# Kernel optimization log

Measured on AMD Instinct MI355X. Metric: run time of the kernel, lower is better.

Reference implementation:

```python
import jax, jax.numpy as jnp
import numpy as np
from jax import lax

B, C_IN, H, W = 32, 128, 64, 64
K, C_OUT, KS = 8, 128, 3
HID = C_IN * 4  # extend = 4
TEMPERATURE = 1.0
PAD = 1


def setup_inputs() -> dict:
    key = jax.random.key(0)
    ks = jax.random.split(key, 7)
    x = jax.random.normal(ks[0], (B, C_IN, H, W), jnp.float32)
    prompt_param = jax.random.uniform(ks[1], (1, K, HID), jnp.float32)
    w1 = jax.random.normal(ks[2], (HID, C_IN), jnp.float32) * 0.05
    b1 = jnp.zeros((HID,), jnp.float32)
    w2 = jax.random.normal(ks[3], (HID, HID), jnp.float32) * 0.05
    b2 = jnp.zeros((HID,), jnp.float32)
    kernels_weights = jax.random.normal(ks[4], (K, C_OUT, C_IN, KS, KS), jnp.float32) * 0.05
    kernels_bias = jax.random.normal(ks[5], (K, C_OUT), jnp.float32) * 0.05
    return {
        'x': x, 'prompt_param': prompt_param,
        'w1': w1, 'b1': b1, 'w2': w2, 'b2': b2,
        'kernels_weights': kernels_weights, 'kernels_bias': kernels_bias,
    }


def reference(x, prompt_param, w1, b1, w2, b2, kernels_weights, kernels_bias):
    # Attention: global avg pool -> MLP -> prompt dot -> softmax over kernels
    pooled = jnp.mean(x, axis=(2, 3))                       # (B, C_in)
    h = jax.nn.relu(pooled @ w1.T + b1)                     # (B, HID)
    s = h @ w2.T + b2                                       # (B, HID)
    scores = jnp.sum(s[:, None, :] * prompt_param, axis=-1)  # (B, K)
    alphas = jax.nn.softmax(scores / TEMPERATURE, axis=-1)   # (B, K)

    # Per-sample kernel aggregation
    agg_w = jnp.einsum('bk,koihw->boihw', alphas, kernels_weights)  # (B,O,I,kh,kw)
    agg_b = alphas @ kernels_bias                                    # (B, O)

    # Per-sample conv2d (equivalent to the groups=B grouped-conv trick)
    def conv_one(xi, wi):
        # xi: (C_in,H,W), wi: (O,C_in,kh,kw)
        return lax.conv_general_dilated(
            xi[None], wi, window_strides=(1, 1),
            padding=((PAD, PAD), (PAD, PAD)),
            dimension_numbers=('NCHW', 'OIHW', 'NCHW'))[0]
    out = jax.vmap(conv_one)(x, agg_w)                       # (B,O,H,W)
    out = out + agg_b[:, :, None, None]
    return out
```

## Files before the change

### kernel.cpp

```cpp
#include <hip/hip_runtime.h>
#include <hip/hip_bf16.h>
#include <stdint.h>


typedef __bf16 v8bf __attribute__((ext_vector_type(8)));
typedef float  v4f  __attribute__((ext_vector_type(4)));

#define XT_OFF     0u
#define XT_BYTES   (32u*4096u*128u*2u)
#define AGGW_OFF   (XT_OFF + XT_BYTES)
#define AGGW_BYTES (32u*9u*128u*128u*2u)
#define PART_OFF   (AGGW_OFF)
#define POOLED_OFF (AGGW_OFF + 0x100000u)
#define H_OFF      (AGGW_OFF + 0x110000u)
#define PSCORE_OFF (AGGW_OFF + 0x120000u)
#define ALPHA_OFF  (AGGW_OFF + AGGW_BYTES)
#define ALPHA_BYTES (32u*8u*4u)
#define AGGB_OFF   (ALPHA_OFF + ALPHA_BYTES)
#define AGGB_BYTES (32u*128u*4u)

typedef const void __attribute__((address_space(1))) gconst_t;
typedef void       __attribute__((address_space(3))) ldsv_t;

__device__ __forceinline__ void g2l16(const void* g, void* l) {
  __builtin_amdgcn_global_load_lds((gconst_t*)g, (ldsv_t*)l, 16, 0, 0);
}

__global__ __launch_bounds__(256) void pool_convert_kernel(
    const float* __restrict__ x, float* __restrict__ partial,
    __hip_bfloat16* __restrict__ xT) {
  const int b = blockIdx.x >> 6;
  const int h = blockIdx.x & 63;
  const int tid = threadIdx.x;
  const int wv = tid >> 6, lane = tid & 63;
  const int wq = lane & 15;
  const int cl = lane >> 4;
  __shared__ __align__(16) __hip_bfloat16 sT[64 * 130];

  const float* xrow = x + (((size_t)b * 128) << 12) + (h << 6);
  #pragma unroll
  for (int i = 0; i < 8; ++i) {
    int c = wv * 32 + i * 4 + cl;
    float4 v = *(const float4*)&xrow[((size_t)c << 12) + wq * 4];
    int w0 = wq * 4;
    sT[(w0 + 0) * 130 + c] = __float2bfloat16(v.x);
    sT[(w0 + 1) * 130 + c] = __float2bfloat16(v.y);
    sT[(w0 + 2) * 130 + c] = __float2bfloat16(v.z);
    sT[(w0 + 3) * 130 + c] = __float2bfloat16(v.w);
    float s = v.x + v.y + v.z + v.w;
    s += __shfl_xor(s, 1);
    s += __shfl_xor(s, 2);
    s += __shfl_xor(s, 4);
    s += __shfl_xor(s, 8);
    if (wq == 0) partial[((b << 6) + h) * 128 + c] = s;
  }
  __syncthreads();
  const int pw = tid >> 2;
  const int piece = tid & 3;
  const uint32_t* s32 = (const uint32_t*)sT;
  uint32_t vals[16];
  #pragma unroll
  for (int j = 0; j < 16; ++j) vals[j] = s32[pw * 65 + piece * 16 + j];
  char* dst = (char*)xT + ((((size_t)b << 6) + h) * 64 + pw) * 256 + piece * 64;
  #pragma unroll
  for (int j = 0; j < 4; ++j)
    ((uint4*)dst)[j] = make_uint4(vals[4*j], vals[4*j+1], vals[4*j+2], vals[4*j+3]);
}

__global__ __launch_bounds__(128) void pool_reduce_kernel(
    const float* __restrict__ partial, float* __restrict__ pooled) {
  const int b = blockIdx.x, c = threadIdx.x;
  float acc = 0.0f;
  const float* src = partial + ((size_t)b << 6) * 128 + c;
  #pragma unroll 8
  for (int h = 0; h < 64; ++h) acc += src[h * 128];
  pooled[b * 128 + c] = acc * (1.0f / 4096.0f);
}

__global__ __launch_bounds__(256) void attn_l1_kernel(
    const float* __restrict__ pooled, const float* __restrict__ w1,
    const float* __restrict__ b1, float* __restrict__ hbuf) {
  const int jt = blockIdx.x * 8;
  const int tid = threadIdx.x;
  __shared__ float sW[8 * 132];
  __shared__ float sPool[32 * 132];

  {
    int r = tid >> 5, c4 = (tid & 31) * 4;
    *(float4*)&sW[r * 132 + c4] = *(const float4*)&w1[(jt + r) * 128 + c4];
  }
  #pragma unroll
  for (int q = 0; q < 4; ++q) {
    int idx = q * 256 + tid;
    int bb = idx >> 5, c4 = (idx & 31) * 4;
    *(float4*)&sPool[bb * 132 + c4] = *(const float4*)&pooled[bb * 128 + c4];
  }
  __syncthreads();

  const int b = tid >> 3, jr = tid & 7;
  float acc = 0.0f;
  #pragma unroll
  for (int i4 = 0; i4 < 32; ++i4) {
    float4 pv = *(const float4*)&sPool[b * 132 + i4 * 4];
    float4 wv = *(const float4*)&sW[jr * 132 + i4 * 4];
    acc += pv.x * wv.x + pv.y * wv.y + pv.z * wv.z + pv.w * wv.w;
  }
  hbuf[b * 512 + jt + jr] = fmaxf(acc + b1[jt + jr], 0.0f);
}

__global__ __launch_bounds__(256) void attn_l2s_kernel(
    const float* __restrict__ hbuf, const float* __restrict__ w2,
    const float* __restrict__ b2, const float* __restrict__ prompt,
    float* __restrict__ pscore) {
  const int jtile = blockIdx.x >> 1;
  const int bg = blockIdx.x & 1;
  const int jt = jtile * 8;
  const int tid = threadIdx.x;
  __shared__ float sW2[8 * 516];
  __shared__ float sH[16 * 516];
  __shared__ float sSc[16 * 9];
  __shared__ float sPr[64];

  #pragma unroll
  for (int q = 0; q < 4; ++q) {
    int idx = q * 256 + tid;
    int r = idx >> 7, c4 = (idx & 127) * 4;
    *(float4*)&sW2[r * 516 + c4] = *(const float4*)&w2[(jt + r) * 512 + c4];
  }
  #pragma unroll
  for (int q = 0; q < 8; ++q) {
    int idx = q * 256 + tid;
    int r = idx >> 7, c4 = (idx & 127) * 4;
    *(float4*)&sH[r * 516 + c4] =
        *(const float4*)&hbuf[(bg * 16 + r) * 512 + c4];
  }
  if (tid < 64) sPr[tid] = prompt[(tid >> 3) * 512 + jt + (tid & 7)];
  __syncthreads();

  const int pair = tid >> 1, half = tid & 1;
  const int bl = pair >> 3, jr = pair & 7;
  float acc = 0.0f;
  #pragma unroll
  for (int i4 = 0; i4 < 64; ++i4) {
    int idx = (half * 64 + i4) * 4;
    float4 hv = *(const float4*)&sH[bl * 516 + idx];
    float4 wv = *(const float4*)&sW2[jr * 516 + idx];
    acc += hv.x * wv.x + hv.y * wv.y + hv.z * wv.z + hv.w * wv.w;
  }
  acc += __shfl_xor(acc, 1);
  if (half == 0) sSc[bl * 9 + jr] = acc + b2[jt + jr];
  __syncthreads();

  if (tid < 128) {
    int bl = tid >> 3, k = tid & 7;
    float p = 0.0f;
    #pragma unroll
    for (int jj = 0; jj < 8; ++jj) p = fmaf(sSc[bl * 9 + jj], sPr[k * 8 + jj], p);
    pscore[((size_t)(jtile * 32 + bg * 16 + bl)) * 8 + k] = p;
  }
}

__global__ __launch_bounds__(256) void softmax_aggb_kernel(
    const float* __restrict__ pscore, const float* __restrict__ kbias,
    float* __restrict__ alphas, float* __restrict__ aggb) {
  const int b = blockIdx.x;
  const int tid = threadIdx.x;
  __shared__ float sRed[32 * 8], sSc[8], sA[8];

  {
    int jt2 = tid >> 3, k = tid & 7;
    sRed[jt2 * 8 + k] = pscore[((size_t)(jt2 * 32 + b)) * 8 + k] +
                        pscore[((size_t)((jt2 + 32) * 32 + b)) * 8 + k];
  }
  __syncthreads();
  if (tid < 8) {
    float sc = 0.0f;
    #pragma unroll
    for (int j = 0; j < 32; ++j) sc += sRed[j * 8 + tid];
    sSc[tid] = sc;
  }
  __syncthreads();
  if (tid == 0) {
    float mx = sSc[0];
    for (int k = 1; k < 8; ++k) mx = fmaxf(mx, sSc[k]);
    float sum = 0.0f, e[8];
    for (int k = 0; k < 8; ++k) { e[k] = expf(sSc[k] - mx); sum += e[k]; }
    float inv = 1.0f / sum;
    for (int k = 0; k < 8; ++k) sA[k] = e[k] * inv;
  }
  __syncthreads();
  if (tid < 8) alphas[b * 8 + tid] = sA[tid];
  if (tid < 128) {
    float acc = 0.0f;
    #pragma unroll
    for (int k = 0; k < 8; ++k) acc = fmaf(sA[k], kbias[k * 128 + tid], acc);
    aggb[b * 128 + tid] = acc;
  }
}

__global__ __launch_bounds__(128) void agg_weights_kernel(
    const float* __restrict__ kw, const float* __restrict__ alphas,
    __hip_bfloat16* __restrict__ aggw) {
  const int co = blockIdx.x;
  const int bg = blockIdx.y;
  const int tid = threadIdx.x;
  __shared__ float sA[64];
  __shared__ float sbuf[1152];
  if (tid < 64) sA[tid] = alphas[bg * 64 + tid];
  __syncthreads();

  float acc[8][9];
  #pragma unroll
  for (int bb = 0; bb < 8; ++bb)
    #pragma unroll
    for (int q = 0; q < 9; ++q) acc[bb][q] = 0.0f;

  for (int k = 0; k < 8; ++k) {
    const float* src = kw + ((size_t)(k * 128 + co)) * 1152;
    float v[9];
    #pragma unroll
    for (int q = 0; q < 9; ++q) v[q] = src[tid + 128 * q];
    #pragma unroll
    for (int bb = 0; bb < 8; ++bb) {
      float a = sA[bb * 8 + k];
      #pragma unroll
      for (int q = 0; q < 9; ++q) acc[bb][q] = fmaf(a, v[q], acc[bb][q]);
    }
  }

  #pragma unroll 1
  for (int bb = 0; bb < 8; ++bb) {
    __syncthreads();
    #pragma unroll
    for (int q = 0; q < 9; ++q) sbuf[tid + 128 * q] = acc[bb][q];
    __syncthreads();
    const int b = bg * 8 + bb;
    #pragma unroll
    for (int t = 0; t < 9; ++t)
      aggw[(((size_t)(b * 9 + t) * 128 + co) << 7) + tid] =
          __float2bfloat16(sbuf[tid * 9 + t]);
  }
}

#define XTILE_B 33792
#define ABUF_B  16384

__global__ __launch_bounds__(256) void dyn_conv_kernel(
    const __hip_bfloat16* __restrict__ xT, const __hip_bfloat16* __restrict__ aggw,
    const float* __restrict__ aggb, float* __restrict__ out) {
  const int tile = blockIdx.x;
  const int b    = blockIdx.y;
  const int tid  = threadIdx.x;
  const int wv = tid >> 6, lane = tid & 63;
  const int wm = wv >> 1, wn = wv & 1;
  const int lm = lane & 15, quad = lane >> 4;
  const int r0 = tile * 2;

  __shared__ __align__(16) char smem[XTILE_B + 2 * ABUF_B + 512];
  char* xb = smem;
  char* abuf = smem + XTILE_B;
  float* sBias = (float*)(smem + XTILE_B + 2 * ABUF_B);

  if (tid < 128) sBias[tid] = aggb[b * 128 + tid];

  for (int pos = tid; pos < 264; pos += 256) {
    int tr = pos / 66, tc = pos - tr * 66;
    int h = r0 - 1 + tr, w = tc - 1;
    if ((unsigned)h >= 64u || (unsigned)w >= 64u) {
      int4* d = (int4*)(xb + pos * 128);
      #pragma unroll
      for (int i = 0; i < 8; ++i) d[i] = make_int4(0, 0, 0, 0);
    }
  }

  const char* xTb = (const char*)xT + ((size_t)b << 20);
  const char* awb = (const char*)aggw + (size_t)b * 294912;

  auto stageX = [&](int half) {
    for (int i = wv; i < 33; i += 4) {
      int P = (i << 6) + lane;
      int pos = P >> 3, slot = P & 7;
      int tr = pos / 66, tc = pos - tr * 66;
      int h = r0 - 1 + tr, w = tc - 1;
      char* dst = xb + (i << 10);
      if ((unsigned)h < 64u && (unsigned)w < 64u) {
        int p = slot ^ (pos & 7);
        const char* src = xTb + (((h << 6) + w) << 8) + (half << 7) + (p << 4);
        g2l16(src, dst);
      }
    }
  };

  auto stageA = [&](int tap, int half) {
    char* ab = abuf + (tap & 1) * ABUF_B;
    #pragma unroll
    for (int sub = 0; sub < 2; ++sub) {
      const int cic = half * 2 + sub;
      const char* base = awb + (tap << 15) + (cic << 6);
      #pragma unroll
      for (int jj = 0; jj < 2; ++jj) {
        int j = wv * 2 + jj;
        int co = (j << 4) + (lane >> 2);
        int f = lane & 3;
        int p = f ^ ((co >> 1) & 3);
        g2l16(base + (co << 8) + (p << 4), ab + sub * 8192 + (j << 10));
      }
    }
  };

  int posb[4];
  #pragma unroll
  for (int ni = 0; ni < 4; ++ni) {
    int n = wn * 64 + ni * 16 + lm;
    posb[ni] = (n >> 6) * 66 + (n & 63);
  }
  const int fA = (quad ^ ((lm >> 1) & 3)) << 4;
  int aoff[4];
  #pragma unroll
  for (int mi = 0; mi < 4; ++mi) {
    int co = wm * 64 + mi * 16 + lm;
    aoff[mi] = (co << 6) + fA;
  }

  v4f acc[4][4];
  #pragma unroll
  for (int mi = 0; mi < 4; ++mi)
    #pragma unroll
    for (int ni = 0; ni < 4; ++ni) acc[mi][ni] = v4f{0.f, 0.f, 0.f, 0.f};

  auto computeTap = [&](int tap) {
    const int th = tap / 3, tw = tap - th * 3;
    const int tapAdd = th * 66 + tw;
    char* ab = abuf + (tap & 1) * ABUF_B;
    #pragma unroll
    for (int sub = 0; sub < 2; ++sub) {
      v8bf af[4], bfr[4];
      #pragma unroll
      for (int mi = 0; mi < 4; ++mi)
        af[mi] = *(const v8bf*)(ab + sub * 8192 + aoff[mi]);
      const int piece = (sub << 2) | quad;
      #pragma unroll
      for (int ni = 0; ni < 4; ++ni) {
        int pos = posb[ni] + tapAdd;
        int pp = (piece ^ (pos & 7)) << 4;
        bfr[ni] = *(const v8bf*)(xb + (pos << 7) + pp);
      }
      #pragma unroll
      for (int mi = 0; mi < 4; ++mi)
        #pragma unroll
        for (int ni = 0; ni < 4; ++ni)
          acc[mi][ni] = __builtin_amdgcn_mfma_f32_16x16x32_bf16(
              af[mi], bfr[ni], acc[mi][ni], 0, 0, 0);
    }
  };

  stageA(0, 0);
  stageA(1, 0);
  stageX(0);
  __syncthreads();
  #pragma unroll
  for (int tap = 0; tap < 9; ++tap) {
    computeTap(tap);
    __syncthreads();
    if (tap + 2 < 9) stageA(tap + 2, 0);
  }
  stageX(1);
  stageA(0, 1);
  stageA(1, 1);
  __syncthreads();
  #pragma unroll
  for (int tap = 0; tap < 9; ++tap) {
    computeTap(tap);
    if (tap < 8) {
      __syncthreads();
      if (tap + 2 < 9) stageA(tap + 2, 1);
    }
  }

  #pragma unroll
  for (int mi = 0; mi < 4; ++mi) {
    #pragma unroll
    for (int r = 0; r < 4; ++r) {
      int co = wm * 64 + mi * 16 + quad * 4 + r;
      float bias = sBias[co];
      #pragma unroll
      for (int ni = 0; ni < 4; ++ni) {
        int n = wn * 64 + ni * 16 + lm;
        out[(((size_t)(b * 128 + co)) << 12) + tile * 128 + n] =
            acc[mi][ni][r] + bias;
      }
    }
  }
}

extern "C" void kernel_launch(void* const* d_in, const int* in_sizes, int n_in,
                              void* d_out, int out_size, void* d_ws, size_t ws_size,
                              hipStream_t stream) {
  const float* x      = (const float*)d_in[0];
  const float* prompt = (const float*)d_in[1];
  const float* w1     = (const float*)d_in[2];
  const float* b1     = (const float*)d_in[3];
  const float* w2     = (const float*)d_in[4];
  const float* b2     = (const float*)d_in[5];
  const float* kw     = (const float*)d_in[6];
  const float* kb     = (const float*)d_in[7];
  float* out = (float*)d_out;
  char* ws = (char*)d_ws;

  __hip_bfloat16* xT   = (__hip_bfloat16*)(ws + XT_OFF);
  __hip_bfloat16* aggw = (__hip_bfloat16*)(ws + AGGW_OFF);
  float* part   = (float*)(ws + PART_OFF);
  float* pooled = (float*)(ws + POOLED_OFF);
  float* hbuf   = (float*)(ws + H_OFF);
  float* pscore = (float*)(ws + PSCORE_OFF);
  float* alphas = (float*)(ws + ALPHA_OFF);
  float* aggb   = (float*)(ws + AGGB_OFF);

  pool_convert_kernel<<<2048, 256, 0, stream>>>(x, part, xT);
  pool_reduce_kernel<<<32, 128, 0, stream>>>(part, pooled);
  attn_l1_kernel<<<64, 256, 0, stream>>>(pooled, w1, b1, hbuf);
  attn_l2s_kernel<<<128, 256, 0, stream>>>(hbuf, w2, b2, prompt, pscore);
  softmax_aggb_kernel<<<32, 256, 0, stream>>>(pscore, kb, alphas, aggb);
  agg_weights_kernel<<<dim3(128, 4), 128, 0, stream>>>(kw, alphas, aggw);
  dyn_conv_kernel<<<dim3(32, 32), 256, 0, stream>>>(xT, aggw, aggb, out);
}
```

Before: 205.7 us.

## Fold prompt into W2, fuse attention chain, hand-sync conv tap pipeline

Uses associativity to precompute prompt·W2 and prompt·b2, so the attention score becomes a dot product of h with a (K,512) matrix. Pooling reduce, layer 1, score, softmax and bias aggregation then fit in one per-sample kernel, replacing four launches. The conv kernel's per-tap __syncthreads is replaced by explicit waitcnt, sched_barrier and raw s_barrier sequences, so loads from the staged prefetch can stay in flight across barriers. The cost is hand-tuned vmcnt counts that must match the number of loads issued per stage, and a prompt precompute kernel that reruns on every call.

```diff
diff --git a/kernel.cpp b/kernel.cpp
--- a/kernel.cpp
+++ b/kernel.cpp
@@ -11,9 +11,8 @@
 #define AGGW_OFF   (XT_OFF + XT_BYTES)
 #define AGGW_BYTES (32u*9u*128u*128u*2u)
 #define PART_OFF   (AGGW_OFF)
-#define POOLED_OFF (AGGW_OFF + 0x100000u)
-#define H_OFF      (AGGW_OFF + 0x110000u)
-#define PSCORE_OFF (AGGW_OFF + 0x120000u)
+#define PP_OFF     (AGGW_OFF + 0x100000u)
+#define PB_OFF     (AGGW_OFF + 0x110000u)
 #define ALPHA_OFF  (AGGW_OFF + AGGW_BYTES)
 #define ALPHA_BYTES (32u*8u*4u)
 #define AGGB_OFF   (ALPHA_OFF + ALPHA_BYTES)
@@ -24,6 +23,30 @@
 
 __device__ __forceinline__ void g2l16(const void* g, void* l) {
   __builtin_amdgcn_global_load_lds((gconst_t*)g, (ldsv_t*)l, 16, 0, 0);
+}
+
+#define VM_WAIT(N)  asm volatile("s_waitcnt vmcnt(" #N ")" ::: "memory")
+#define LGKM_WAIT0() asm volatile("s_waitcnt lgkmcnt(0)" ::: "memory")
+#define SCHED_FENCE() __builtin_amdgcn_sched_barrier(0)
+#define RAW_BARRIER() __builtin_amdgcn_s_barrier()
+
+__global__ __launch_bounds__(512) void prompt_pre_kernel(
+    const float* __restrict__ prompt, const float* __restrict__ w2,
+    const float* __restrict__ b2, float* __restrict__ pp,
+    float* __restrict__ pb) {
+  const int k = blockIdx.x, i = threadIdx.x;
+  __shared__ float sP[512];
+  sP[i] = prompt[k * 512 + i];
+  __syncthreads();
+  float acc = 0.0f;
+  #pragma unroll 8
+  for (int j = 0; j < 512; ++j) acc = fmaf(sP[j], w2[j * 512 + i], acc);
+  pp[k * 512 + i] = acc;
+  if (i == 0) {
+    float a = 0.0f;
+    for (int j = 0; j < 512; ++j) a = fmaf(sP[j], b2[j], a);
+    pb[k] = a;
+  }
 }
 
 __global__ __launch_bounds__(256) void pool_convert_kernel(
@@ -67,124 +90,66 @@
     ((uint4*)dst)[j] = make_uint4(vals[4*j], vals[4*j+1], vals[4*j+2], vals[4*j+3]);
 }
 
-__global__ __launch_bounds__(128) void pool_reduce_kernel(
-    const float* __restrict__ partial, float* __restrict__ pooled) {
-  const int b = blockIdx.x, c = threadIdx.x;
-  float acc = 0.0f;
-  const float* src = partial + ((size_t)b << 6) * 128 + c;
-  #pragma unroll 8
-  for (int h = 0; h < 64; ++h) acc += src[h * 128];
-  pooled[b * 128 + c] = acc * (1.0f / 4096.0f);
-}
-
-__global__ __launch_bounds__(256) void attn_l1_kernel(
-    const float* __restrict__ pooled, const float* __restrict__ w1,
-    const float* __restrict__ b1, float* __restrict__ hbuf) {
-  const int jt = blockIdx.x * 8;
-  const int tid = threadIdx.x;
-  __shared__ float sW[8 * 132];
-  __shared__ float sPool[32 * 132];
+__global__ __launch_bounds__(256) void attn_fused_kernel(
+    const float* __restrict__ partial, const float* __restrict__ w1,
+    const float* __restrict__ b1, const float* __restrict__ pp,
+    const float* __restrict__ pb, const float* __restrict__ kbias,
+    float* __restrict__ alphas, float* __restrict__ aggb) {
+  const int b = blockIdx.x, tid = threadIdx.x;
+  __shared__ float sTmp[256];
+  __shared__ float sPool[128];
+  __shared__ float sH[512];
+  __shared__ float sS[8], sA[8];
 
   {
-    int r = tid >> 5, c4 = (tid & 31) * 4;
-    *(float4*)&sW[r * 132 + c4] = *(const float4*)&w1[(jt + r) * 128 + c4];
-  }
-  #pragma unroll
-  for (int q = 0; q < 4; ++q) {
-    int idx = q * 256 + tid;
-    int bb = idx >> 5, c4 = (idx & 31) * 4;
-    *(float4*)&sPool[bb * 132 + c4] = *(const float4*)&pooled[bb * 128 + c4];
-  }
-  __syncthreads();
-
-  const int b = tid >> 3, jr = tid & 7;
-  float acc = 0.0f;
-  #pragma unroll
-  for (int i4 = 0; i4 < 32; ++i4) {
-    float4 pv = *(const float4*)&sPool[b * 132 + i4 * 4];
-    float4 wv = *(const float4*)&sW[jr * 132 + i4 * 4];
-    acc += pv.x * wv.x + pv.y * wv.y + pv.z * wv.z + pv.w * wv.w;
-  }
-  hbuf[b * 512 + jt + jr] = fmaxf(acc + b1[jt + jr], 0.0f);
-}
-
-__global__ __launch_bounds__(256) void attn_l2s_kernel(
-    const float* __restrict__ hbuf, const float* __restrict__ w2,
-    const float* __restrict__ b2, const float* __restrict__ prompt,
-    float* __restrict__ pscore) {
-  const int jtile = blockIdx.x >> 1;
-  const int bg = blockIdx.x & 1;
-  const int jt = jtile * 8;
-  const int tid = threadIdx.x;
-  __shared__ float sW2[8 * 516];
-  __shared__ float sH[16 * 516];
-  __shared__ float sSc[16 * 9];
-  __shared__ float sPr[64];
-
-  #pragma unroll
-  for (int q = 0; q < 4; ++q) {
-    int idx = q * 256 + tid;
-    int r = idx >> 7, c4 = (idx & 127) * 4;
-    *(float4*)&sW2[r * 516 + c4] = *(const float4*)&w2[(jt + r) * 512 + c4];
-  }
-  #pragma unroll
-  for (int q = 0; q < 8; ++q) {
-    int idx = q * 256 + tid;
-    int r = idx >> 7, c4 = (idx & 127) * 4;
-    *(float4*)&sH[r * 516 + c4] =
-        *(const float4*)&hbuf[(bg * 16 + r) * 512 + c4];
-  }
-  if (tid < 64) sPr[tid] = prompt[(tid >> 3) * 512 + jt + (tid & 7)];
-  __syncthreads();
-
-  const int pair = tid >> 1, half = tid & 1;
-  const int bl = pair >> 3, jr = pair & 7;
-  float acc = 0.0f;
-  #pragma unroll
-  for (int i4 = 0; i4 < 64; ++i4) {
-    int idx = (half * 64 + i4) * 4;
-    float4 hv = *(const float4*)&sH[bl * 516 + idx];
-    float4 wv = *(const float4*)&sW2[jr * 516 + idx];
-    acc += hv.x * wv.x + hv.y * wv.y + hv.z * wv.z + hv.w * wv.w;
-  }
-  acc += __shfl_xor(acc, 1);
-  if (half == 0) sSc[bl * 9 + jr] = acc + b2[jt + jr];
-  __syncthreads();
-
-  if (tid < 128) {
-    int bl = tid >> 3, k = tid & 7;
-    float p = 0.0f;
-    #pragma unroll
-    for (int jj = 0; jj < 8; ++jj) p = fmaf(sSc[bl * 9 + jj], sPr[k * 8 + jj], p);
-    pscore[((size_t)(jtile * 32 + bg * 16 + bl)) * 8 + k] = p;
-  }
-}
-
-__global__ __launch_bounds__(256) void softmax_aggb_kernel(
-    const float* __restrict__ pscore, const float* __restrict__ kbias,
-    float* __restrict__ alphas, float* __restrict__ aggb) {
-  const int b = blockIdx.x;
-  const int tid = threadIdx.x;
-  __shared__ float sRed[32 * 8], sSc[8], sA[8];
+    const int c = tid & 127, hh = tid >> 7;
+    const float* src = partial + ((size_t)b << 6) * 128 + hh * 128 + c;
+    float acc = 0.0f;
+    #pragma unroll
+    for (int h2 = 0; h2 < 32; ++h2) acc += src[h2 * 256];
+    sTmp[tid] = acc;
+  }
+  __syncthreads();
+  if (tid < 128) sPool[tid] = (sTmp[tid] + sTmp[tid + 128]) * (1.0f / 4096.0f);
+  __syncthreads();
+
+  #pragma unroll
+  for (int q = 0; q < 2; ++q) {
+    const int j = q * 256 + tid;
+    const float* wr = w1 + j * 128;
+    float acc = 0.0f;
+    #pragma unroll
+    for (int i4 = 0; i4 < 32; ++i4) {
+      float4 wv = *(const float4*)&wr[i4 * 4];
+      acc += wv.x * sPool[i4*4] + wv.y * sPool[i4*4+1] +
+             wv.z * sPool[i4*4+2] + wv.w * sPool[i4*4+3];
+    }
+    sH[j] = fmaxf(acc + b1[j], 0.0f);
+  }
+  __syncthreads();
 
   {
-    int jt2 = tid >> 3, k = tid & 7;
-    sRed[jt2 * 8 + k] = pscore[((size_t)(jt2 * 32 + b)) * 8 + k] +
-                        pscore[((size_t)((jt2 + 32) * 32 + b)) * 8 + k];
-  }
-  __syncthreads();
-  if (tid < 8) {
-    float sc = 0.0f;
-    #pragma unroll
-    for (int j = 0; j < 32; ++j) sc += sRed[j * 8 + tid];
-    sSc[tid] = sc;
-  }
-  __syncthreads();
+    const int k = tid >> 5, seg = tid & 31;
+    const float* ppk = pp + k * 512 + seg * 16;
+    const float* hk  = sH + seg * 16;
+    float acc = 0.0f;
+    #pragma unroll
+    for (int t4 = 0; t4 < 4; ++t4) {
+      float4 pv = *(const float4*)&ppk[t4 * 4];
+      acc += pv.x * hk[t4*4] + pv.y * hk[t4*4+1] +
+             pv.z * hk[t4*4+2] + pv.w * hk[t4*4+3];
+    }
+    #pragma unroll
+    for (int m = 16; m > 0; m >>= 1) acc += __shfl_xor(acc, m);
+    if (seg == 0) sS[k] = acc + pb[k];
+  }
+  __syncthreads();
+
   if (tid == 0) {
-    float mx = sSc[0];
-    for (int k = 1; k < 8; ++k) mx = fmaxf(mx, sSc[k]);
+    float mx = sS[0];
+    for (int k = 1; k < 8; ++k) mx = fmaxf(mx, sS[k]);
     float sum = 0.0f, e[8];
-    for (int k = 0; k < 8; ++k) { e[k] = expf(sSc[k] - mx); sum += e[k]; }
+    for (int k = 0; k < 8; ++k) { e[k] = expf(sS[k] - mx); sum += e[k]; }
     float inv = 1.0f / sum;
     for (int k = 0; k < 8; ++k) sA[k] = e[k] * inv;
   }
@@ -354,28 +319,32 @@
     }
   };
 
+  #define TAP_STEP(t, half)                                            \
+    computeTap(t);                                                     \
+    if ((t) < 8) {                                                     \
+      LGKM_WAIT0(); SCHED_FENCE();                                     \
+      RAW_BARRIER(); SCHED_FENCE();                                    \
+      if ((t) + 2 < 9) { stageA((t) + 2, half); VM_WAIT(4); }          \
+      else             { VM_WAIT(0); }                                 \
+      SCHED_FENCE();                                                   \
+      RAW_BARRIER(); SCHED_FENCE();                                    \
+    }
+
   stageA(0, 0);
   stageA(1, 0);
   stageX(0);
   __syncthreads();
-  #pragma unroll
-  for (int tap = 0; tap < 9; ++tap) {
-    computeTap(tap);
-    __syncthreads();
-    if (tap + 2 < 9) stageA(tap + 2, 0);
-  }
+  TAP_STEP(0, 0) TAP_STEP(1, 0) TAP_STEP(2, 0) TAP_STEP(3, 0) TAP_STEP(4, 0)
+  TAP_STEP(5, 0) TAP_STEP(6, 0) TAP_STEP(7, 0) TAP_STEP(8, 0)
+  LGKM_WAIT0(); SCHED_FENCE();
+  __syncthreads();
   stageX(1);
   stageA(0, 1);
   stageA(1, 1);
   __syncthreads();
-  #pragma unroll
-  for (int tap = 0; tap < 9; ++tap) {
-    computeTap(tap);
-    if (tap < 8) {
-      __syncthreads();
-      if (tap + 2 < 9) stageA(tap + 2, 1);
-    }
-  }
+  TAP_STEP(0, 1) TAP_STEP(1, 1) TAP_STEP(2, 1) TAP_STEP(3, 1) TAP_STEP(4, 1)
+  TAP_STEP(5, 1) TAP_STEP(6, 1) TAP_STEP(7, 1) TAP_STEP(8, 1)
+  #undef TAP_STEP
 
   #pragma unroll
   for (int mi = 0; mi < 4; ++mi) {
@@ -410,17 +379,15 @@
   __hip_bfloat16* xT   = (__hip_bfloat16*)(ws + XT_OFF);
   __hip_bfloat16* aggw = (__hip_bfloat16*)(ws + AGGW_OFF);
   float* part   = (float*)(ws + PART_OFF);
-  float* pooled = (float*)(ws + POOLED_OFF);
-  float* hbuf   = (float*)(ws + H_OFF);
-  float* pscore = (float*)(ws + PSCORE_OFF);
+  float* pp     = (float*)(ws + PP_OFF);
+  float* pb     = (float*)(ws + PB_OFF);
   float* alphas = (float*)(ws + ALPHA_OFF);
   float* aggb   = (float*)(ws + AGGB_OFF);
 
+  prompt_pre_kernel<<<8, 512, 0, stream>>>(prompt, w2, b2, pp, pb);
   pool_convert_kernel<<<2048, 256, 0, stream>>>(x, part, xT);
-  pool_reduce_kernel<<<32, 128, 0, stream>>>(part, pooled);
-  attn_l1_kernel<<<64, 256, 0, stream>>>(pooled, w1, b1, hbuf);
-  attn_l2s_kernel<<<128, 256, 0, stream>>>(hbuf, w2, b2, prompt, pscore);
-  softmax_aggb_kernel<<<32, 256, 0, stream>>>(pscore, kb, alphas, aggb);
+  attn_fused_kernel<<<32, 256, 0, stream>>>(part, w1, b1, pp, pb, kb,
+                                            alphas, aggb);
   agg_weights_kernel<<<dim3(128, 4), 128, 0, stream>>>(kw, alphas, aggw);
   dyn_conv_kernel<<<dim3(32, 32), 256, 0, stream>>>(xT, aggw, aggb, out);
 }
```

Measured after the change: 246.2 us. 19.7% more time.
